# Performance work log

Measured on AMD Instinct MI355X. Metric: run time of the kernel, lower is better.

## Reference

```python
import jax, jax.numpy as jnp
import numpy as np
import math

D = 192            # base channel dim (init arg d); s has D channels
D2 = 2 * D         # y has 2d channels
H = 48; W = 48; BS = 2
NH = 8             # attention heads (divides both D2 and D)
NY = H * W         # tokens per image


def pe2d(d_model, height, width):
    """Faithful port of positionalencoding2d: (d_model, H, W)."""
    dh = d_model // 2
    div = jnp.exp(jnp.arange(0.0, dh, 2.0) * (-math.log(10000.0) / dh))  # (dh/2,)
    pw = jnp.arange(0.0, width)[:, None] * div    # (W, dh/2)
    ph = jnp.arange(0.0, height)[:, None] * div   # (H, dh/2)
    pe = jnp.zeros((d_model, height, width), jnp.float32)
    pe = pe.at[0:dh:2].set(jnp.broadcast_to(jnp.sin(pw).T[:, None, :], (dh // 2, height, width)))
    pe = pe.at[1:dh:2].set(jnp.broadcast_to(jnp.cos(pw).T[:, None, :], (dh // 2, height, width)))
    pe = pe.at[dh::2].set(jnp.broadcast_to(jnp.sin(ph).T[:, :, None], (dh // 2, height, width)))
    pe = pe.at[dh + 1::2].set(jnp.broadcast_to(jnp.cos(ph).T[:, :, None], (dh // 2, height, width)))
    return pe


def conv1x1(x, w, b):
    # x: (b,c,h,w), w: (out,c)
    return jnp.einsum('bchw,oc->bohw', x, w) + b[None, :, None, None]


def conv3x3(x, w, b):
    out = jax.lax.conv_general_dilated(x, w, (1, 1), 'SAME',
                                       dimension_numbers=('NCHW', 'OIHW', 'NCHW'))
    return out + b[None, :, None, None]


def bn(x, g, b):
    # inference-mode batchnorm with zero-mean / unit-var running stats
    return x * g[None, :, None, None] + b[None, :, None, None]


def setup_inputs() -> dict:
    key = jax.random.key(0)
    ks = jax.random.split(key, 8)
    r = lambda k, shp: jax.random.normal(k, shp, jnp.float32) * 0.02
    return {
        'y': jax.random.normal(ks[0], (BS, D2, H, W), jnp.float32),
        's': jax.random.normal(ks[1], (BS, D, H, W), jnp.float32),
        'wq_w': r(ks[2], (D2, D2)), 'wq_b': jnp.zeros((D2,), jnp.float32),
        'wk_w': r(ks[3], (D2, D2)), 'wk_b': jnp.zeros((D2,), jnp.float32),
        'wv_w': r(ks[4], (D, D)),   'wv_b': jnp.zeros((D,), jnp.float32),
        'conv1_w': r(ks[5], (D2, D2)), 'conv1_b': jnp.zeros((D2,), jnp.float32),
        'bn1_g': jnp.ones((D2,), jnp.float32), 'bn1_b': jnp.zeros((D2,), jnp.float32),
        'conv2_w': r(ks[6], (D, D)), 'conv2_b': jnp.zeros((D,), jnp.float32),
        'bn2_g': jnp.ones((D,), jnp.float32), 'bn2_b': jnp.zeros((D,), jnp.float32),
        'up_w': r(ks[7], (D2, D2, 3, 3)), 'up_b': jnp.zeros((D2,), jnp.float32),
        'conv3_w': r(jax.random.fold_in(key, 10), (D, D2)), 'conv3_b': jnp.zeros((D,), jnp.float32),
        'bn3_g': jnp.ones((D,), jnp.float32), 'bn3_b': jnp.zeros((D,), jnp.float32),
        'sig_w': r(jax.random.fold_in(key, 11), (D, D)), 'sig_b': jnp.zeros((D,), jnp.float32),
        'bnsig_g': jnp.ones((D,), jnp.float32), 'bnsig_b': jnp.zeros((D,), jnp.float32),
    }


def reference(y, s, wq_w, wq_b, wk_w, wk_b, wv_w, wv_b,
              conv1_w, conv1_b, bn1_g, bn1_b,
              conv2_w, conv2_b, bn2_g, bn2_b,
              up_w, up_b, conv3_w, conv3_b, bn3_g, bn3_b,
              sig_w, sig_b, bnsig_g, bnsig_b):
    bs = y.shape[0]
    y = y + pe2d(D2, H, W)[None]
    s = s + pe2d(D, H, W)[None]
    # conv+BN+ReLU feature extraction
    y_c1 = jax.nn.relu(bn(conv1x1(y, conv1_w, conv1_b), bn1_g, bn1_b))
    s_c2 = jax.nn.relu(bn(conv1x1(s, conv2_w, conv2_b), bn2_g, bn2_b))
    y_c3 = conv3x3(y, up_w, up_b)                                   # 'up' branch conv
    y_c3 = jax.nn.relu(bn(conv1x1(y_c3, conv3_w, conv3_b), bn3_g, bn3_b))  # (b, D, H, W)
    # tokenize
    yt = y_c1.reshape(bs, D2, NY).transpose(0, 2, 1)   # (b, ny, 2d)
    st = s_c2.reshape(bs, D, NY).transpose(0, 2, 1)    # (b, ny, d)
    # multi-head cross attention: Q,K from y-tokens, V from s-tokens
    Q = (yt @ wq_w.T + wq_b).reshape(bs, NY, NH, D2 // NH).transpose(0, 2, 1, 3)  # (b,h,ny,2d/h)
    K = (yt @ wk_w.T + wk_b).reshape(bs, NY, NH, D2 // NH).transpose(0, 2, 1, 3)
    V = (st @ wv_w.T + wv_b).reshape(bs, NY, NH, D // NH).transpose(0, 2, 1, 3)   # (b,h,ny,d/h)
    M = jnp.einsum('bhnd,bhmd->bhnm', Q, K) / math.sqrt(D)  # scale = d**0.5 as in source
    A = jax.nn.softmax(M, axis=-1)
    Z = jnp.einsum('bhnm,bhmd->bhnd', A, V)                 # (b,h,ny,d/h)
    Z = Z.transpose(0, 2, 1, 3).reshape(bs, NY, D).transpose(0, 2, 1).reshape(bs, D, H, W)
    # sigmoid gate and fuse
    g = jax.nn.sigmoid(bn(conv1x1(Z, sig_w, sig_b), bnsig_g, bnsig_b))
    Z = g * s
    return jnp.concatenate([Z, y_c3], axis=1)               # (b, 2d, H, W)
```

## Files before the change

### kernel.cpp

```cpp
#include <hip/hip_runtime.h>
#include <hip/hip_bf16.h>

#define Dc   192
#define D2c  384
#define NYc  2304

#define QSCALE 0.1041175462f

typedef __attribute__((ext_vector_type(8))) short short8;
typedef __attribute__((ext_vector_type(4))) float f32x4;

__device__ __forceinline__ unsigned short f2bf(float f) {
    unsigned int u = __float_as_uint(f);
    u += 0x7FFFu + ((u >> 16) & 1u);
    return (unsigned short)(u >> 16);
}
__device__ __forceinline__ float fexp2(float x) {
    float r; asm("v_exp_f32 %0, %1" : "=v"(r) : "v"(x)); return r;
}
__device__ __forceinline__ unsigned cvtpk(float lo, float hi) {
    unsigned r; asm("v_cvt_pk_bf16_f32 %0, %1, %2" : "=v"(r) : "v"(lo), "v"(hi));
    return r;
}

__global__ __launch_bounds__(256)
void build_pe_kernel(float* __restrict__ peY, float* __restrict__ peS) {
    int idx = blockIdx.x * 256 + threadIdx.x;
    int c, p, C; float* dst; int off;
    if (idx < 18432) { c = idx / 48; p = idx % 48; C = 384; dst = peY; off = idx; }
    else { int k = idx - 18432; c = k / 48; p = k % 48; C = 192; dst = peS; off = k; }
    int dh = C >> 1;
    int i = ((c < dh) ? c : c - dh) >> 1;
    float divv = expf((float)(2 * i) * (-9.210340371976184f / (float)dh));
    float ang = (float)p * divv;
    dst[off] = (c & 1) ? cosf(ang) : sinf(ang);
}

__global__ __launch_bounds__(256)
void prep_pe_kernel(const float* __restrict__ y, const float* __restrict__ s,
                    const float* __restrict__ peY, const float* __restrict__ peS,
                    unsigned short* __restrict__ ytok, unsigned short* __restrict__ stok,
                    float* __restrict__ sch) {
    int idx = blockIdx.x * 256 + threadIdx.x;
    if (idx < 1769472) {
        int n = idx % NYc; int c = (idx / NYc) % D2c; int b = idx / (NYc * D2c);
        int pos = (c < 192) ? (n % 48) : (n / 48);
        float v = y[idx] + peY[c * 48 + pos];
        ytok[(long)b * NYc * D2c + (long)n * D2c + c] = f2bf(v);
    } else {
        int k = idx - 1769472;
        int n = k % NYc; int c = (k / NYc) % Dc; int b = k / (NYc * Dc);
        int pos = (c < 96) ? (n % 48) : (n / 48);
        float v = s[k] + peS[c * 48 + pos];
        sch[k] = v;
        stok[(long)b * NYc * Dc + (long)n * Dc + c] = f2bf(v);
    }
}

__global__ __launch_bounds__(256)
void prep_w_kernel(const float* __restrict__ w0, const float* __restrict__ w1,
                   const float* __restrict__ w2, const float* __restrict__ w3,
                   const float* __restrict__ w4, const float* __restrict__ w5,
                   const float* __restrict__ w6, unsigned short* __restrict__ dst,
                   const float* __restrict__ wq_b, const float* __restrict__ wk_b,
                   float* __restrict__ qkb,
                   const float* __restrict__ upw, unsigned short* __restrict__ upwt) {
    int idx = blockIdx.x * 256 + threadIdx.x;
    if (idx < 626688) {
        if (idx < 768)
            qkb[idx] = (idx < 384) ? wq_b[idx] * QSCALE : wk_b[idx - 384];
        const float* src; int off; float scl = 1.0f;
        if      (idx < 147456) { src = w0; off = idx; }
        else if (idx < 294912) { src = w1; off = idx - 147456; scl = QSCALE; }
        else if (idx < 442368) { src = w2; off = idx - 294912; }
        else if (idx < 479232) { src = w3; off = idx - 442368; }
        else if (idx < 516096) { src = w4; off = idx - 479232; }
        else if (idx < 552960) { src = w5; off = idx - 516096; }
        else                   { src = w6; off = idx - 552960; }
        dst[idx] = f2bf(src[off] * scl);
    } else {
        int k = idx - 626688;
        int o = k / 3456; int r = k % 3456;
        int tap = r / 384;  int c = r % 384;
        upwt[k] = f2bf(upw[((long)o * 384 + c) * 9 + tap]);
    }
}

enum { E_BIAS = 0, E_BNRELU = 1, E_BNRELU_F32 = 2, E_SIG_F32 = 3 };

template<int EPI, bool IM2COL, bool CH_M, int BMt, int BNt>
__global__ __launch_bounds__(256)
void mfma_gemm(const unsigned short* __restrict__ Ar, long aBatch, int aPitch,
               const unsigned short* __restrict__ Br, long bBatch, int bPitch,
               int K,
               const float* __restrict__ bias, const float* __restrict__ bng,
               const float* __restrict__ bnb,
               const float* __restrict__ smul, long smulBatch,
               void* __restrict__ outv, long oBatch, int oPitch)
{
    constexpr int MF = BMt / 32;
    constexpr int NF = BNt / 32;
    constexpr int LA = BMt / 32;
    constexpr int LB = BNt / 32;

    int b = blockIdx.z;
    const unsigned short* A = Ar + (long)b * aBatch;
    const unsigned short* B = Br + (long)b * bBatch;
    int m0 = blockIdx.x * BMt, n0 = blockIdx.y * BNt;

    __shared__ __align__(16) unsigned short As[BMt][72];
    __shared__ __align__(16) unsigned short Bs[BNt][72];

    int t = threadIdx.x, lane = t & 63, w = t >> 6;
    int lr = lane & 15, lg = lane >> 4;
    int wm = (BMt == 128) ? (w >> 1) * 64 : (w & 1) * 32;
    int wn = (BNt == 128) ? (w >> 1) * 64 : (w & 1) * 32;

    f32x4 acc[MF][NF];
    #pragma unroll
    for (int i = 0; i < MF; ++i)
        #pragma unroll
        for (int j = 0; j < NF; ++j)
            acc[i][j] = (f32x4){0.f, 0.f, 0.f, 0.f};

    uint4 ra[LA], rb[LB];

    auto load = [&](int k0) {
        #pragma unroll
        for (int i = 0; i < LA; ++i) {
            int idx = t + i * 256, row = idx >> 3, sl = idx & 7;
            if (!IM2COL) {
                ra[i] = *(const uint4*)(A + (long)(m0 + row) * aPitch + k0 + sl * 8);
            } else {
                int tok = m0 + row;
                int bb = (tok >= NYc) ? 1 : 0;
                int n = tok - bb * NYc;
                int tap = k0 / 384;
                int rem = k0 - tap * 384 + sl * 8;
                int py = n / 48 + tap / 3 - 1;
                int px = n % 48 + tap % 3 - 1;
                ra[i] = (py >= 0 && py < 48 && px >= 0 && px < 48)
                    ? *(const uint4*)(A + ((long)bb * NYc + py * 48 + px) * aPitch + rem)
                    : make_uint4(0, 0, 0, 0);
            }
        }
        #pragma unroll
        for (int i = 0; i < LB; ++i) {
            int idx = t + i * 256, row = idx >> 3, sl = idx & 7;
            rb[i] = *(const uint4*)(B + (long)(n0 + row) * bPitch + k0 + sl * 8);
        }
    };
    auto store = [&]() {
        #pragma unroll
        for (int i = 0; i < LA; ++i) {
            int idx = t + i * 256;
            *(uint4*)&As[idx >> 3][(idx & 7) * 8] = ra[i];
        }
        #pragma unroll
        for (int i = 0; i < LB; ++i) {
            int idx = t + i * 256;
            *(uint4*)&Bs[idx >> 3][(idx & 7) * 8] = rb[i];
        }
    };

    load(0); store(); __syncthreads();

    int NT = K / 64;
    for (int tt = 0; tt < NT; ++tt) {
        if (tt + 1 < NT) load((tt + 1) * 64);
        #pragma unroll
        for (int kk = 0; kk < 2; ++kk) {
            short8 af[MF], bf[NF];
            #pragma unroll
            for (int i = 0; i < MF; ++i)
                af[i] = *(const short8*)&As[wm + i * 16 + lr][kk * 32 + lg * 8];
            #pragma unroll
            for (int j = 0; j < NF; ++j)
                bf[j] = *(const short8*)&Bs[wn + j * 16 + lr][kk * 32 + lg * 8];
            #pragma unroll
            for (int i = 0; i < MF; ++i)
                #pragma unroll
                for (int j = 0; j < NF; ++j)
                    acc[i][j] = __builtin_amdgcn_mfma_f32_16x16x32_bf16(
                                    af[i], bf[j], acc[i][j], 0, 0, 0);
        }
        __syncthreads();
        if (tt + 1 < NT) { store(); __syncthreads(); }
    }

    float* outF = (float*)outv;
    unsigned short* outH = (unsigned short*)outv;
    long ob = (long)b * oBatch;
    #pragma unroll
    for (int i = 0; i < MF; ++i)
    #pragma unroll
    for (int j = 0; j < NF; ++j)
    #pragma unroll
    for (int r = 0; r < 4; ++r) {
        int gm = m0 + wm + i * 16 + lg * 4 + r;
        int gn = n0 + wn + j * 16 + lr;
        int ch = CH_M ? gm : gn;
        float v = acc[i][j][r] + bias[ch];
        if (EPI == E_BNRELU || EPI == E_BNRELU_F32)
            v = fmaxf(fmaf(v, bng[ch], bnb[ch]), 0.f);
        if (EPI == E_SIG_F32) {
            v = fmaf(v, bng[ch], bnb[ch]);
            v = 1.f / (1.f + __expf(-v));
            v *= smul[(long)b * smulBatch + (long)gm * NYc + gn];
        }
        long o = ob + (long)gm * oPitch + gn;
        if (EPI == E_BNRELU_F32 || EPI == E_SIG_F32) outF[o] = v;
        else                                         outH[o] = f2bf(v);
    }
}

__global__ __launch_bounds__(512)
void attn_kernel(const unsigned short* __restrict__ QK,
                 const unsigned short* __restrict__ Vc,
                 unsigned short* __restrict__ Zt)
{
    int qb = blockIdx.x;
    int bh = blockIdx.y;
    int b = bh >> 3, h = bh & 7;
    const unsigned short* Qg = QK + (long)b * NYc * 768 + h * 48;
    const unsigned short* Kg = Qg + 384;
    const unsigned short* Vg = Vc + ((long)b * Dc + h * 24) * NYc;
    unsigned short*       Z  = Zt + (long)b * NYc * Dc + h * 24;

    __shared__ __align__(16) unsigned short Ks_[128][72];
    __shared__ __align__(16) unsigned short Vs_[32][136];
    __shared__ __align__(16) unsigned int   Ps_[8][16][36];

    int t = threadIdx.x, lane = t & 63, w = t >> 6;
    int lr = lane & 15, lg = lane >> 4;
    int tm = w >> 1, hf = w & 1;
    int q0 = qb * 64;

    short8 z8 = {0, 0, 0, 0, 0, 0, 0, 0};
    const unsigned short* qrow = Qg + (long)(q0 + tm * 16 + lr) * 768;
    short8 bq0 = *(const short8*)(qrow + lg * 8);
    short8 bq1 = (lg < 2) ? *(const short8*)(qrow + 32 + lg * 8) : z8;

    float m_run = -1e30f, l_run = 0.f;
    f32x4 O0 = {0.f, 0.f, 0.f, 0.f}, O1 = {0.f, 0.f, 0.f, 0.f};

    for (int kt = 0; kt < 18; ++kt) {
        long k0 = kt * 128;
        #pragma unroll
        for (int i = 0; i < 2; ++i) {
            int idx = t + i * 512;
            int row = idx >> 3, sl = idx & 7;
            uint4 v = make_uint4(0, 0, 0, 0);
            if (sl < 6) v = *(const uint4*)(Kg + (k0 + row) * 768 + sl * 8);
            *(uint4*)&Ks_[row][sl * 8] = v;
        }
        if (t < 384) {
            int row = t >> 4, sl = t & 15;
            *(uint4*)&Vs_[row][sl * 8] =
                *(const uint4*)(Vg + (long)row * NYc + k0 + sl * 8);
        }
        __syncthreads();

        f32x4 sS[4];
        #pragma unroll
        for (int ks = 0; ks < 4; ++ks) {
            short8 ak0 = *(const short8*)&Ks_[hf * 64 + ks * 16 + lr][lg * 8];
            short8 ak1 = *(const short8*)&Ks_[hf * 64 + ks * 16 + lr][32 + lg * 8];
            f32x4 c = {0.f, 0.f, 0.f, 0.f};
            c = __builtin_amdgcn_mfma_f32_16x16x32_bf16(ak0, bq0, c, 0, 0, 0);
            c = __builtin_amdgcn_mfma_f32_16x16x32_bf16(ak1, bq1, c, 0, 0, 0);
            sS[ks] = c;
        }

        float tmax = -1e30f;
        #pragma unroll
        for (int ks = 0; ks < 4; ++ks)
            #pragma unroll
            for (int r = 0; r < 4; ++r) tmax = fmaxf(tmax, sS[ks][r]);
        tmax = fmaxf(tmax, __shfl_xor(tmax, 16));
        tmax = fmaxf(tmax, __shfl_xor(tmax, 32));

        if (__any(tmax > m_run + 10.f)) {
            float mn = fmaxf(m_run, tmax);
            float al = fexp2(m_run - mn);
            m_run = mn;
            l_run *= al;
            #pragma unroll
            for (int rr = 0; rr < 4; ++rr) {
                float arr = __shfl(al, (lane & 48) | (lg * 4 + rr));
                O0[rr] *= arr; O1[rr] *= arr;
            }
        }

        float psum = 0.f;
        #pragma unroll
        for (int ks = 0; ks < 4; ++ks) {
            float p0 = fexp2(sS[ks][0] - m_run);
            float p1 = fexp2(sS[ks][1] - m_run);
            float p2 = fexp2(sS[ks][2] - m_run);
            float p3 = fexp2(sS[ks][3] - m_run);
            psum += (p0 + p1) + (p2 + p3);
            Ps_[w][lr][8 * ks + 2 * lg]     = cvtpk(p0, p1);
            Ps_[w][lr][8 * ks + 2 * lg + 1] = cvtpk(p2, p3);
        }
        psum += __shfl_xor(psum, 16);
        psum += __shfl_xor(psum, 32);
        l_run += psum;

        short8 ap0 = *(const short8*)&Ps_[w][lr][4 * lg];
        short8 ap1 = *(const short8*)&Ps_[w][lr][16 + 4 * lg];
        short8 bv00 = *(const short8*)&Vs_[lr][hf * 64 + lg * 8];
        short8 bv01 = *(const short8*)&Vs_[lr][hf * 64 + 32 + lg * 8];
        short8 bv10 = *(const short8*)&Vs_[16 + lr][hf * 64 + lg * 8];
        short8 bv11 = *(const short8*)&Vs_[16 + lr][hf * 64 + 32 + lg * 8];
        O0 = __builtin_amdgcn_mfma_f32_16x16x32_bf16(ap0, bv00, O0, 0, 0, 0);
        O0 = __builtin_amdgcn_mfma_f32_16x16x32_bf16(ap1, bv01, O0, 0, 0, 0);
        O1 = __builtin_amdgcn_mfma_f32_16x16x32_bf16(ap0, bv10, O1, 0, 0, 0);
        O1 = __builtin_amdgcn_mfma_f32_16x16x32_bf16(ap1, bv11, O1, 0, 0, 0);
        __syncthreads();
    }

    float* Cf = (float*)&Ps_[0][0][0];
    float* T = Cf + tm * 576;
    if (hf == 1) {
        #pragma unroll
        for (int j = 0; j < 4; ++j) {
            T[lane * 8 + j]     = O0[j];
            T[lane * 8 + 4 + j] = O1[j];
        }
        if (lane < 16) { T[512 + lane] = m_run; T[528 + lane] = l_run; }
    }
    __syncthreads();
    if (hf == 0) {
        float mB = T[512 + lr], lB = T[528 + lr];
        float mS = fmaxf(m_run, mB);
        float aA = fexp2(m_run - mS), aB = fexp2(mB - mS);
        float invl = 1.f / (l_run * aA + lB * aB);
        float fA = aA * invl, fB = aB * invl;
        #pragma unroll
        for (int rr = 0; rr < 4; ++rr) {
            int src = (lane & 48) | (lg * 4 + rr);
            float gA = __shfl(fA, src), gB = __shfl(fB, src);
            int n = q0 + tm * 16 + lg * 4 + rr;
            unsigned short* zr = Z + (long)n * Dc;
            float z0 = O0[rr] * gA + T[lane * 8 + rr] * gB;
            zr[lr] = f2bf(z0);
            if (lr < 8) {
                float z1 = O1[rr] * gA + T[lane * 8 + 4 + rr] * gB;
                zr[16 + lr] = f2bf(z1);
            }
        }
    }
}

extern "C" void kernel_launch(void* const* d_in, const int* in_sizes, int n_in,
                              void* d_out, int out_size, void* d_ws, size_t ws_size,
                              hipStream_t stream) {
    const float* y       = (const float*)d_in[0];
    const float* s       = (const float*)d_in[1];
    const float* wq_w    = (const float*)d_in[2];
    const float* wq_b    = (const float*)d_in[3];
    const float* wk_w    = (const float*)d_in[4];
    const float* wk_b    = (const float*)d_in[5];
    const float* wv_w    = (const float*)d_in[6];
    const float* wv_b    = (const float*)d_in[7];
    const float* conv1_w = (const float*)d_in[8];
    const float* conv1_b = (const float*)d_in[9];
    const float* bn1_g   = (const float*)d_in[10];
    const float* bn1_b   = (const float*)d_in[11];
    const float* conv2_w = (const float*)d_in[12];
    const float* conv2_b = (const float*)d_in[13];
    const float* bn2_g   = (const float*)d_in[14];
    const float* bn2_b   = (const float*)d_in[15];
    const float* up_w    = (const float*)d_in[16];
    const float* up_b    = (const float*)d_in[17];
    const float* conv3_w = (const float*)d_in[18];
    const float* conv3_b = (const float*)d_in[19];
    const float* bn3_g   = (const float*)d_in[20];
    const float* bn3_b   = (const float*)d_in[21];
    const float* sig_w   = (const float*)d_in[22];
    const float* sig_b   = (const float*)d_in[23];
    const float* bnsig_g = (const float*)d_in[24];
    const float* bnsig_b = (const float*)d_in[25];

    unsigned short* wsp   = (unsigned short*)d_ws;
    unsigned short* wcvt  = wsp;
    unsigned short* upwt  = wcvt + 626688;
    unsigned short* y_pe  = upwt + 1327104;
    unsigned short* s_pe  = y_pe + 1769472;
    unsigned short* y_c1  = s_pe + 884736;
    unsigned short* s_c2  = y_c1 + 1769472;
    unsigned short* y_up  = s_c2 + 884736;
    unsigned short* QKtok = y_up + 1769472;
    unsigned short* Vch   = QKtok + 3538944;
    unsigned short* Ztok  = Vch + 884736;
    float*          s_ch  = (float*)(Ztok + 884736);
    float*          qkb   = s_ch + 884736;
    float*          peY   = qkb + 768;
    float*          peS   = peY + 18432;

    const unsigned short* conv1wb = wcvt;
    const unsigned short* wqkb    = wcvt + 147456;
    const unsigned short* conv2wb = wcvt + 442368;
    const unsigned short* wvb     = wcvt + 479232;
    const unsigned short* sigwb   = wcvt + 516096;
    const unsigned short* conv3wb = wcvt + 552960;

    const long SY2 = (long)D2c * NYc;
    const long SY1 = (long)Dc * NYc;

    build_pe_kernel<<<108, 256, 0, stream>>>(peY, peS);
    prep_pe_kernel<<<10368, 256, 0, stream>>>(y, s, peY, peS, y_pe, s_pe, s_ch);
    prep_w_kernel<<<7632, 256, 0, stream>>>(conv1_w, wq_w, wk_w, conv2_w,
                                            wv_w, sig_w, conv3_w, wcvt,
                                            wq_b, wk_b, qkb, up_w, upwt);

    dim3 blk(256);
    mfma_gemm<E_BNRELU, false, false, 128, 64><<<dim3(36, 6, 1), blk, 0, stream>>>(
        y_pe, 0, D2c, conv1wb, 0, D2c, D2c,
        conv1_b, bn1_g, bn1_b, nullptr, 0, y_c1, 0, D2c);
    mfma_gemm<E_BNRELU, false, false, 128, 64><<<dim3(36, 3, 1), blk, 0, stream>>>(
        s_pe, 0, Dc, conv2wb, 0, Dc, Dc,
        conv2_b, bn2_g, bn2_b, nullptr, 0, s_c2, 0, Dc);
    mfma_gemm<E_BIAS, true, false, 128, 64><<<dim3(36, 6, 1), blk, 0, stream>>>(
        y_pe, 0, D2c, upwt, 0, 9 * D2c, 9 * D2c,
        up_b, nullptr, nullptr, nullptr, 0, y_up, 0, D2c);
    mfma_gemm<E_BNRELU_F32, false, true, 64, 128><<<dim3(3, 18, 2), blk, 0, stream>>>(
        conv3wb, 0, D2c, y_up, SY2, D2c, D2c,
        conv3_b, bn3_g, bn3_b, nullptr, 0,
        (float*)d_out + (long)Dc * NYc, SY2, NYc);
    mfma_gemm<E_BIAS, false, false, 128, 64><<<dim3(36, 12, 1), blk, 0, stream>>>(
        y_c1, 0, D2c, wqkb, 0, D2c, D2c,
        qkb, nullptr, nullptr, nullptr, 0, QKtok, 0, 768);
    mfma_gemm<E_BIAS, false, true, 64, 128><<<dim3(3, 18, 2), blk, 0, stream>>>(
        wvb, 0, Dc, s_c2, SY1, Dc, Dc,
        wv_b, nullptr, nullptr, nullptr, 0, Vch, SY1, NYc);
    attn_kernel<<<dim3(36, 16), dim3(512), 0, stream>>>(QKtok, Vch, Ztok);
    mfma_gemm<E_SIG_F32, false, true, 64, 128><<<dim3(3, 18, 2), blk, 0, stream>>>(
        sigwb, 0, Dc, Ztok, SY1, Dc, Dc,
        sig_b, bnsig_g, bnsig_b, s_ch, SY1,
        (float*)d_out, SY2, NYc);
}
```

Baseline: 226.8 us.

## Group independent GEMMs into segmented launches, tile-transpose PE prep, swizzle block order

Replaces the per-GEMM templated launches with a segmented fused_gemm kernel. Each block picks its segment descriptor from its block id, so independent GEMMs (conv1/conv2/up-conv, then QK/conv3/V) run in one launch each. The block shape becomes a uniform 64x64 tile. The prep kernel now transposes through a shared-memory tile so both the global reads and the token-major bf16 writes are coalesced. An XCD-aware block swizzle is added to both the GEMMs and attention. Launch count and tail effects should drop. The costs are smaller tiles with less reuse, and epilogue flags that are runtime branches instead of template constants.

```diff
diff --git a/kernel.cpp b/kernel.cpp
--- a/kernel.cpp
+++ b/kernel.cpp
@@ -21,6 +21,9 @@
 __device__ __forceinline__ unsigned cvtpk(float lo, float hi) {
     unsigned r; asm("v_cvt_pk_bf16_f32 %0, %1, %2" : "=v"(r) : "v"(lo), "v"(hi));
     return r;
+}
+__device__ __forceinline__ int swz8(int bid, int nwg) {
+    return (bid & 7) * (nwg >> 3) + (bid >> 3);
 }
 
 __global__ __launch_bounds__(256)
@@ -41,19 +44,35 @@
                     const float* __restrict__ peY, const float* __restrict__ peS,
                     unsigned short* __restrict__ ytok, unsigned short* __restrict__ stok,
                     float* __restrict__ sch) {
-    int idx = blockIdx.x * 256 + threadIdx.x;
-    if (idx < 1769472) {
-        int n = idx % NYc; int c = (idx / NYc) % D2c; int b = idx / (NYc * D2c);
-        int pos = (c < 192) ? (n % 48) : (n / 48);
-        float v = y[idx] + peY[c * 48 + pos];
-        ytok[(long)b * NYc * D2c + (long)n * D2c + c] = f2bf(v);
-    } else {
-        int k = idx - 1769472;
-        int n = k % NYc; int c = (k / NYc) % Dc; int b = k / (NYc * Dc);
-        int pos = (c < 96) ? (n % 48) : (n / 48);
-        float v = s[k] + peS[c * 48 + pos];
-        sch[k] = v;
-        stok[(long)b * NYc * Dc + (long)n * Dc + c] = f2bf(v);
+    __shared__ unsigned short T[64][66];
+    int bid = blockIdx.x;
+    int b, ct, nt, C; const float* in; const float* pe; unsigned short* outp; bool isS;
+    if (bid < 432) { isS = false; b = bid / 216; int r = bid % 216; ct = r / 36; nt = r % 36;
+                     in = y; pe = peY; outp = ytok; C = 384; }
+    else { int l = bid - 432; isS = true; b = l / 108; int r = l % 108; ct = r / 36; nt = r % 36;
+           in = s; pe = peS; outp = stok; C = 192; }
+    int t = threadIdx.x;
+    int nl = t & 63;
+    int n = nt * 64 + nl;
+    int pos_x = n % 48, pos_y = n / 48;
+    #pragma unroll
+    for (int i = 0; i < 16; ++i) {
+        int cl = (t >> 6) + 4 * i;
+        int c = ct * 64 + cl;
+        int pos = (c < (C >> 1)) ? pos_x : pos_y;
+        long gi = (long)b * C * NYc + (long)c * NYc + n;
+        float v = in[gi] + pe[c * 48 + pos];
+        if (isS) sch[gi] = v;
+        T[nl][cl] = f2bf(v);
+    }
+    __syncthreads();
+    #pragma unroll
+    for (int i = 0; i < 8; ++i) {
+        int nl2 = (t >> 5) + 8 * i;
+        int cp  = t & 31;
+        unsigned u = (unsigned)T[nl2][2 * cp] | ((unsigned)T[nl2][2 * cp + 1] << 16);
+        long row = (long)b * NYc + nt * 64 + nl2;
+        *(unsigned*)(outp + row * C + ct * 64 + 2 * cp) = u;
     }
 }
 
@@ -86,131 +105,117 @@
     }
 }
 
-enum { E_BIAS = 0, E_BNRELU = 1, E_BNRELU_F32 = 2, E_SIG_F32 = 3 };
-
-template<int EPI, bool IM2COL, bool CH_M, int BMt, int BNt>
+struct Seg {
+    const unsigned short* A; const unsigned short* B;
+    int aP, bP, K, nT, blkOff, flags;
+    const float *bias, *bng, *bnb;
+    char* out; int oPitch; long oBatch;
+};
+
+template<int NSEG>
 __global__ __launch_bounds__(256)
-void mfma_gemm(const unsigned short* __restrict__ Ar, long aBatch, int aPitch,
-               const unsigned short* __restrict__ Br, long bBatch, int bPitch,
-               int K,
-               const float* __restrict__ bias, const float* __restrict__ bng,
-               const float* __restrict__ bnb,
-               const float* __restrict__ smul, long smulBatch,
-               void* __restrict__ outv, long oBatch, int oPitch)
+void fused_gemm(Seg s0, Seg s1, Seg s2, const float* __restrict__ smul)
 {
-    constexpr int MF = BMt / 32;
-    constexpr int NF = BNt / 32;
-    constexpr int LA = BMt / 32;
-    constexpr int LB = BNt / 32;
-
-    int b = blockIdx.z;
-    const unsigned short* A = Ar + (long)b * aBatch;
-    const unsigned short* B = Br + (long)b * bBatch;
-    int m0 = blockIdx.x * BMt, n0 = blockIdx.y * BNt;
-
-    __shared__ __align__(16) unsigned short As[BMt][72];
-    __shared__ __align__(16) unsigned short Bs[BNt][72];
+    int bid = swz8(blockIdx.x, gridDim.x);
+    Seg sg = s0;
+    if (NSEG > 1 && bid >= s1.blkOff) sg = s1;
+    if (NSEG > 2 && bid >= s2.blkOff) sg = s2;
+    int local = bid - sg.blkOff;
+    int mt = local / sg.nT, nt = local - mt * sg.nT;
+    int m0 = mt * 64, n0 = nt * 64;
+
+    __shared__ __align__(16) unsigned short As[64][72];
+    __shared__ __align__(16) unsigned short Bs[64][72];
 
     int t = threadIdx.x, lane = t & 63, w = t >> 6;
     int lr = lane & 15, lg = lane >> 4;
-    int wm = (BMt == 128) ? (w >> 1) * 64 : (w & 1) * 32;
-    int wn = (BNt == 128) ? (w >> 1) * 64 : (w & 1) * 32;
-
-    f32x4 acc[MF][NF];
-    #pragma unroll
-    for (int i = 0; i < MF; ++i)
-        #pragma unroll
-        for (int j = 0; j < NF; ++j)
+    int wm = (w >> 1) * 32, wn = (w & 1) * 32;
+
+    f32x4 acc[2][2];
+    #pragma unroll
+    for (int i = 0; i < 2; ++i)
+        #pragma unroll
+        for (int j = 0; j < 2; ++j)
             acc[i][j] = (f32x4){0.f, 0.f, 0.f, 0.f};
 
-    uint4 ra[LA], rb[LB];
+    uint4 ra[2], rb[2];
+    bool im2col = (sg.flags & 1) != 0;
 
     auto load = [&](int k0) {
         #pragma unroll
-        for (int i = 0; i < LA; ++i) {
+        for (int i = 0; i < 2; ++i) {
             int idx = t + i * 256, row = idx >> 3, sl = idx & 7;
-            if (!IM2COL) {
-                ra[i] = *(const uint4*)(A + (long)(m0 + row) * aPitch + k0 + sl * 8);
-            } else {
+            if (im2col) {
                 int tok = m0 + row;
-                int bb = (tok >= NYc) ? 1 : 0;
+                int bb = tok >= NYc;
                 int n = tok - bb * NYc;
                 int tap = k0 / 384;
                 int rem = k0 - tap * 384 + sl * 8;
                 int py = n / 48 + tap / 3 - 1;
                 int px = n % 48 + tap % 3 - 1;
                 ra[i] = (py >= 0 && py < 48 && px >= 0 && px < 48)
-                    ? *(const uint4*)(A + ((long)bb * NYc + py * 48 + px) * aPitch + rem)
+                    ? *(const uint4*)(sg.A + ((long)bb * NYc + py * 48 + px) * sg.aP + rem)
                     : make_uint4(0, 0, 0, 0);
+            } else {
+                ra[i] = *(const uint4*)(sg.A + (long)(m0 + row) * sg.aP + k0 + sl * 8);
             }
-        }
-        #pragma unroll
-        for (int i = 0; i < LB; ++i) {
-            int idx = t + i * 256, row = idx >> 3, sl = idx & 7;
-            rb[i] = *(const uint4*)(B + (long)(n0 + row) * bPitch + k0 + sl * 8);
+            rb[i] = *(const uint4*)(sg.B + (long)(n0 + row) * sg.bP + k0 + sl * 8);
         }
     };
     auto store = [&]() {
         #pragma unroll
-        for (int i = 0; i < LA; ++i) {
+        for (int i = 0; i < 2; ++i) {
             int idx = t + i * 256;
             *(uint4*)&As[idx >> 3][(idx & 7) * 8] = ra[i];
-        }
-        #pragma unroll
-        for (int i = 0; i < LB; ++i) {
-            int idx = t + i * 256;
             *(uint4*)&Bs[idx >> 3][(idx & 7) * 8] = rb[i];
         }
     };
 
     load(0); store(); __syncthreads();
-
-    int NT = K / 64;
+    int NT = sg.K >> 6;
     for (int tt = 0; tt < NT; ++tt) {
-        if (tt + 1 < NT) load((tt + 1) * 64);
+        if (tt + 1 < NT) load((tt + 1) << 6);
         #pragma unroll
         for (int kk = 0; kk < 2; ++kk) {
-            short8 af[MF], bf[NF];
-            #pragma unroll
-            for (int i = 0; i < MF; ++i)
-                af[i] = *(const short8*)&As[wm + i * 16 + lr][kk * 32 + lg * 8];
-            #pragma unroll
-            for (int j = 0; j < NF; ++j)
-                bf[j] = *(const short8*)&Bs[wn + j * 16 + lr][kk * 32 + lg * 8];
-            #pragma unroll
-            for (int i = 0; i < MF; ++i)
-                #pragma unroll
-                for (int j = 0; j < NF; ++j)
-                    acc[i][j] = __builtin_amdgcn_mfma_f32_16x16x32_bf16(
-                                    af[i], bf[j], acc[i][j], 0, 0, 0);
+            short8 a0 = *(const short8*)&As[wm + lr][kk * 32 + lg * 8];
+            short8 a1 = *(const short8*)&As[wm + 16 + lr][kk * 32 + lg * 8];
+            short8 b0 = *(const short8*)&Bs[wn + lr][kk * 32 + lg * 8];
+            short8 b1 = *(const short8*)&Bs[wn + 16 + lr][kk * 32 + lg * 8];
+            acc[0][0] = __builtin_amdgcn_mfma_f32_16x16x32_bf16(a0, b0, acc[0][0], 0, 0, 0);
+            acc[0][1] = __builtin_amdgcn_mfma_f32_16x16x32_bf16(a0, b1, acc[0][1], 0, 0, 0);
+            acc[1][0] = __builtin_amdgcn_mfma_f32_16x16x32_bf16(a1, b0, acc[1][0], 0, 0, 0);
+            acc[1][1] = __builtin_amdgcn_mfma_f32_16x16x32_bf16(a1, b1, acc[1][1], 0, 0, 0);
         }
         __syncthreads();
         if (tt + 1 < NT) { store(); __syncthreads(); }
     }
 
-    float* outF = (float*)outv;
-    unsigned short* outH = (unsigned short*)outv;
-    long ob = (long)b * oBatch;
-    #pragma unroll
-    for (int i = 0; i < MF; ++i)
-    #pragma unroll
-    for (int j = 0; j < NF; ++j)
+    #pragma unroll
+    for (int i = 0; i < 2; ++i)
+    #pragma unroll
+    for (int j = 0; j < 2; ++j)
     #pragma unroll
     for (int r = 0; r < 4; ++r) {
         int gm = m0 + wm + i * 16 + lg * 4 + r;
         int gn = n0 + wn + j * 16 + lr;
-        int ch = CH_M ? gm : gn;
-        float v = acc[i][j][r] + bias[ch];
-        if (EPI == E_BNRELU || EPI == E_BNRELU_F32)
-            v = fmaxf(fmaf(v, bng[ch], bnb[ch]), 0.f);
-        if (EPI == E_SIG_F32) {
-            v = fmaf(v, bng[ch], bnb[ch]);
+        int ch = (sg.flags & 8) ? gm : gn;
+        float v = acc[i][j][r] + sg.bias[ch];
+        if (sg.flags & 2)
+            v = fmaxf(fmaf(v, sg.bng[ch], sg.bnb[ch]), 0.f);
+        long o; int b = 0, tok = gn;
+        if (sg.flags & 8) {
+            b = gn >= NYc; tok = gn - b * NYc;
+            o = (long)b * sg.oBatch + (long)gm * sg.oPitch + tok;
+        } else {
+            o = (long)gm * sg.oPitch + gn;
+        }
+        if (sg.flags & 16) {
+            v = fmaf(v, sg.bng[ch], sg.bnb[ch]);
             v = 1.f / (1.f + __expf(-v));
-            v *= smul[(long)b * smulBatch + (long)gm * NYc + gn];
-        }
-        long o = ob + (long)gm * oPitch + gn;
-        if (EPI == E_BNRELU_F32 || EPI == E_SIG_F32) outF[o] = v;
-        else                                         outH[o] = f2bf(v);
+            v *= smul[(long)b * 442368 + (long)gm * NYc + tok];
+        }
+        if (sg.flags & 4) ((float*)sg.out)[o] = v;
+        else              ((unsigned short*)sg.out)[o] = f2bf(v);
     }
 }
 
@@ -219,8 +224,9 @@
                  const unsigned short* __restrict__ Vc,
                  unsigned short* __restrict__ Zt)
 {
-    int qb = blockIdx.x;
-    int bh = blockIdx.y;
+    int nid = swz8(blockIdx.x, 576);
+    int qb = nid % 36;
+    int bh = nid / 36;
     int b = bh >> 3, h = bh & 7;
     const unsigned short* Qg = QK + (long)b * NYc * 768 + h * 48;
     const unsigned short* Kg = Qg + 384;
@@ -406,38 +412,37 @@
     const unsigned short* sigwb   = wcvt + 516096;
     const unsigned short* conv3wb = wcvt + 552960;
 
-    const long SY2 = (long)D2c * NYc;
-    const long SY1 = (long)Dc * NYc;
-
     build_pe_kernel<<<108, 256, 0, stream>>>(peY, peS);
-    prep_pe_kernel<<<10368, 256, 0, stream>>>(y, s, peY, peS, y_pe, s_pe, s_ch);
     prep_w_kernel<<<7632, 256, 0, stream>>>(conv1_w, wq_w, wk_w, conv2_w,
                                             wv_w, sig_w, conv3_w, wcvt,
                                             wq_b, wk_b, qkb, up_w, upwt);
-
-    dim3 blk(256);
-    mfma_gemm<E_BNRELU, false, false, 128, 64><<<dim3(36, 6, 1), blk, 0, stream>>>(
-        y_pe, 0, D2c, conv1wb, 0, D2c, D2c,
-        conv1_b, bn1_g, bn1_b, nullptr, 0, y_c1, 0, D2c);
-    mfma_gemm<E_BNRELU, false, false, 128, 64><<<dim3(36, 3, 1), blk, 0, stream>>>(
-        s_pe, 0, Dc, conv2wb, 0, Dc, Dc,
-        conv2_b, bn2_g, bn2_b, nullptr, 0, s_c2, 0, Dc);
-    mfma_gemm<E_BIAS, true, false, 128, 64><<<dim3(36, 6, 1), blk, 0, stream>>>(
-        y_pe, 0, D2c, upwt, 0, 9 * D2c, 9 * D2c,
-        up_b, nullptr, nullptr, nullptr, 0, y_up, 0, D2c);
-    mfma_gemm<E_BNRELU_F32, false, true, 64, 128><<<dim3(3, 18, 2), blk, 0, stream>>>(
-        conv3wb, 0, D2c, y_up, SY2, D2c, D2c,
-        conv3_b, bn3_g, bn3_b, nullptr, 0,
-        (float*)d_out + (long)Dc * NYc, SY2, NYc);
-    mfma_gemm<E_BIAS, false, false, 128, 64><<<dim3(36, 12, 1), blk, 0, stream>>>(
-        y_c1, 0, D2c, wqkb, 0, D2c, D2c,
-        qkb, nullptr, nullptr, nullptr, 0, QKtok, 0, 768);
-    mfma_gemm<E_BIAS, false, true, 64, 128><<<dim3(3, 18, 2), blk, 0, stream>>>(
-        wvb, 0, Dc, s_c2, SY1, Dc, Dc,
-        wv_b, nullptr, nullptr, nullptr, 0, Vch, SY1, NYc);
-    attn_kernel<<<dim3(36, 16), dim3(512), 0, stream>>>(QKtok, Vch, Ztok);
-    mfma_gemm<E_SIG_F32, false, true, 64, 128><<<dim3(3, 18, 2), blk, 0, stream>>>(
-        sigwb, 0, Dc, Ztok, SY1, Dc, Dc,
-        sig_b, bnsig_g, bnsig_b, s_ch, SY1,
-        (float*)d_out, SY2, NYc);
-}
+    prep_pe_kernel<<<648, 256, 0, stream>>>(y, s, peY, peS, y_pe, s_pe, s_ch);
+
+    Seg sz = {};
+
+    {
+        Seg a = { y_pe, conv1wb, D2c, D2c, D2c, 6, 0, 2,
+                  conv1_b, bn1_g, bn1_b, (char*)y_c1, D2c, 0 };
+        Seg b = { s_pe, conv2wb, Dc, Dc, Dc, 3, 432, 2,
+                  conv2_b, bn2_g, bn2_b, (char*)s_c2, Dc, 0 };
+        Seg c = { y_pe, upwt, D2c, 9 * D2c, 9 * D2c, 6, 648, 1,
+                  up_b, nullptr, nullptr, (char*)y_up, D2c, 0 };
+        fused_gemm<3><<<1080, 256, 0, stream>>>(a, b, c, nullptr);
+    }
+    {
+        Seg a = { y_c1, wqkb, D2c, D2c, D2c, 12, 0, 0,
+                  qkb, nullptr, nullptr, (char*)QKtok, 768, 0 };
+        Seg b = { conv3wb, y_up, D2c, D2c, D2c, 72, 864, 2 | 4 | 8,
+                  conv3_b, bn3_g, bn3_b,
+                  (char*)((float*)d_out + (long)Dc * NYc), NYc, 884736 };
+        Seg c = { wvb, s_c2, Dc, Dc, Dc, 72, 1080, 8,
+                  wv_b, nullptr, nullptr, (char*)Vch, NYc, 442368 };
+        fused_gemm<3><<<1296, 256, 0, stream>>>(a, b, c, nullptr);
+    }
+    attn_kernel<<<576, 512, 0, stream>>>(QKtok, Vch, Ztok);
+    {
+        Seg a = { sigwb, Ztok, Dc, Dc, Dc, 72, 0, 4 | 8 | 16,
+                  sig_b, bnsig_g, bnsig_b, (char*)d_out, NYc, 884736 };
+        fused_gemm<1><<<216, 256, 0, stream>>>(a, sz, sz, s_ch);
+    }
+}
```

New measurement: 287.5 us. +26.8%, slower.
